# Kernel optimization log

Measured on AMD Instinct MI355X. Metric: run time of the kernel, lower is better.

Reference implementation:

```python
import jax, jax.numpy as jnp
import numpy as np

NB_STEPS = 50
ALPHA = 0.9
NUM_RNN_STEPS = 2
B = 4096
NUM_FEATURE = 100
IN_D = 5
HIDDEN = [64, 64, 64]
P1 = (1.1, 1.1, 1.5, 2.0, 2.5)   # IntegrandNN_outer_level powers
P2 = (1.5, 2.0, 2.5, 3.0, 3.5)   # IntegrandNN powers


def _cc(nb_steps):
    # Clenshaw-Curtis weights/steps, identical to UMNN's compute_cc_weights
    n = nb_steps
    i = np.arange(n + 1, dtype=np.float64).reshape(-1, 1)
    lam = np.cos(i @ i.T * np.pi / n)
    lam[:, 0] = 0.5
    lam[:, -1] *= 0.5
    lam = lam * 2.0 / n
    W = np.zeros(n + 1)
    even = np.arange(0, n + 1, 2)
    W[even] = 2.0 / (1.0 - even.astype(np.float64) ** 2)
    W[0] = 1.0
    ccw = (lam.T @ W).astype(np.float32)                         # [n+1]
    steps = np.cos(np.arange(n + 1) * np.pi / n).astype(np.float32)  # [n+1]
    return jnp.asarray(ccw), jnp.asarray(steps)

CC_W, CC_S = _cc(NB_STEPS)


def _mlp(xh, Ws, bs):
    # Linear+ReLU stack with ELU on the last layer (ReLU popped, ELU appended)
    h = xh
    for W, b in zip(Ws[:-1], bs[:-1]):
        h = jax.nn.relu(h @ W.T + b)
    return jax.nn.elu(h @ Ws[-1].T + bs[-1])


def _integrand(x, h, Ws, bs, Wf, powers):
    z = _mlp(jnp.concatenate([x, h], axis=1), Ws, bs) + 1.0      # [N,1], z >= 0
    feats = jnp.concatenate([z ** p for p in powers], axis=1)    # [N,5]
    return jax.nn.relu((1.0 / (feats + 1.0)) @ Wf.T)             # [N,1]


def _integrate(x0, xT, h, f):
    # ParallelNeuralIntegral forward: CC quadrature of f from x0 to xT
    Bn, S = x0.shape[0], NB_STEPS + 1
    X = x0[:, None, :] + (xT - x0)[:, None, :] * (CC_S[None, :, None] + 1.0) / 2.0  # [B,S,1]
    hs = jnp.broadcast_to(h[:, None, :], (Bn, S, h.shape[1])).reshape(-1, h.shape[1])
    dz = f(X.reshape(-1, 1), hs).reshape(Bn, S, 1)
    return (dz * CC_W[None, :, None]).sum(1) * (xT - x0) / 2.0   # [B,1]


def setup_inputs() -> dict:
    key = jax.random.key(0)
    ks = jax.random.split(key, 24)
    def lin(k, o, i):
        return jax.random.normal(k, (o, i), jnp.float32) / np.sqrt(i)
    d = {}
    d["x_"] = jax.random.normal(ks[0], (B, NUM_FEATURE), jnp.float32)
    d["h_"] = jax.random.normal(ks[1], (B, IN_D - 1), jnp.float32)
    d["log_weight"] = jnp.ones((1, NUM_FEATURE), jnp.float32)     # reset_parameters -> 1
    d["sigmoid_param"] = jnp.zeros((1,), jnp.float32)
    sizes = [IN_D] + HIDDEN + [1]
    for tag, base in (("f1", 2), ("f2", 12)):
        for li, (i, o) in enumerate(zip(sizes[:-1], sizes[1:])):
            d[f"{tag}_W{li}"] = lin(ks[base + 2 * li], o, i)
            d[f"{tag}_b{li}"] = jnp.zeros((o,), jnp.float32)
        d[f"{tag}_Wf"] = jnp.abs(lin(ks[base + 9], 1, 5))         # reset_params -> abs
    return d


def reference(x_, h_, log_weight, sigmoid_param,
              f1_W0, f1_b0, f1_W1, f1_b1, f1_W2, f1_b2, f1_W3, f1_b3, f1_Wf,
              f2_W0, f2_b0, f2_W1, f2_b1, f2_W2, f2_b2, f2_W3, f2_b3, f2_Wf):
    f1Ws = [f1_W0, f1_W1, f1_W2, f1_W3]; f1bs = [f1_b0, f1_b1, f1_b2, f1_b3]
    f2Ws = [f2_W0, f2_W1, f2_W2, f2_W3]; f2bs = [f2_b0, f2_b1, f2_b2, f2_b3]
    f1 = lambda x, h: _integrand(x, h, f1Ws, f1bs, f1_Wf, P1)
    f2 = lambda x, h: _integrand(x, h, f2Ws, f2bs, f2_Wf, P2)

    # modular function: linear to [B,1] then sum over dim 1 -> [B,1]
    xm = jnp.sum(x_ * log_weight[0], axis=1, keepdims=True)
    lam = jax.nn.sigmoid(sigmoid_param[0])

    I1 = jnp.zeros_like(xm)
    I2 = jnp.zeros_like(xm)
    out_first = None
    for _ in range(NUM_RNN_STEPS):
        x = (1.0 - lam) * xm + lam * I1
        x2 = (1.0 - lam) * xm + lam * I2
        out_first = f1(x2, h_)
        I1 = _integrate(jnp.zeros_like(x), x, h_, f1)
        xmax = jnp.max(x2) + 10.0
        xfinal = jnp.zeros_like(x) + xmax
        I2 = (1.0 / ALPHA) * _integrate(x2, xfinal, h_, f2)
    return I1, out_first, I2
```

## Files before the change

### kernel.cpp

```cpp
#include <hip/hip_runtime.h>
#include <math.h>

typedef _Float16 half8v __attribute__((ext_vector_type(8)));
typedef _Float16 half4v __attribute__((ext_vector_type(4)));
typedef _Float16 half2v __attribute__((ext_vector_type(2)));
typedef float float4v __attribute__((ext_vector_type(4)));

#define BB    4096
#define INV_ALPHA (1.0f/0.9f)

#define WS_CCW  0
#define WS_CCS  64
#define WS_LAM  128
#define WS_PM16 160
#define WS_PM   256
#define WS_XM   512
#define WS_X    (WS_XM + BB)
#define WS_X2   (WS_X + BB)
#define WS_H    16384
#define H_NET   8192
#define H_W2    4096
#define H_W0    16384
#define H_W3    20480

#if defined(__has_builtin)
#if __has_builtin(__builtin_amdgcn_rcpf)
#define FRCP(x) __builtin_amdgcn_rcpf(x)
#endif
#if __has_builtin(__builtin_amdgcn_exp2f)
#define FEXP2(x) __builtin_amdgcn_exp2f(x)
#endif
#if __has_builtin(__builtin_amdgcn_logf)
#define FLOG2(x) __builtin_amdgcn_logf(x)
#endif
#endif
#ifndef FRCP
#define FRCP(x) (1.0f / (x))
#endif
#ifndef FEXP2
#define FEXP2(x) exp2f(x)
#endif
#ifndef FLOG2
#define FLOG2(x) log2f(x)
#endif

__device__ __forceinline__ int swz(int row, int cb) {
    return (row << 6) + (((cb ^ (row & 7)) & 7) << 3);
}

__device__ __forceinline__ half4v pk_relu4(float4v c) {
#if defined(__has_builtin) && __has_builtin(__builtin_amdgcn_cvt_pkrtz)
    half2v a = __builtin_bit_cast(half2v,
        __builtin_amdgcn_cvt_pkrtz(fmaxf(c[0], 0.0f), fmaxf(c[1], 0.0f)));
    half2v b = __builtin_bit_cast(half2v,
        __builtin_amdgcn_cvt_pkrtz(fmaxf(c[2], 0.0f), fmaxf(c[3], 0.0f)));
    half4v o; o[0] = a[0]; o[1] = a[1]; o[2] = b[0]; o[3] = b[1];
    return o;
#else
    half4v o;
    o[0] = (_Float16)fmaxf(c[0], 0.0f); o[1] = (_Float16)fmaxf(c[1], 0.0f);
    o[2] = (_Float16)fmaxf(c[2], 0.0f); o[3] = (_Float16)fmaxf(c[3], 0.0f);
    return o;
#endif
}

__global__ void k_setup(const float* __restrict__ x_, const float* __restrict__ lw,
                        const float* __restrict__ sp,
                        const float* __restrict__ f1W0, const float* __restrict__ f1W1,
                        const float* __restrict__ f1W2, const float* __restrict__ f1W3,
                        const float* __restrict__ f2W0, const float* __restrict__ f2W1,
                        const float* __restrict__ f2W2, const float* __restrict__ f2W3,
                        float* __restrict__ ws, float* __restrict__ out) {
    _Float16* wh = (_Float16*)(ws + WS_H);
    const int blk = blockIdx.x, tid = threadIdx.x;
    if (blk < 256) {
        int wave = tid >> 6, lane = tid & 63;
        float vmax = -1e30f;
        for (int r = 0; r < 4; ++r) {
            int row = blk * 16 + wave * 4 + r;
            float v = 0.0f;
            for (int i = lane; i < 100; i += 64) v = fmaf(x_[row * 100 + i], lw[i], v);
            #pragma unroll
            for (int off = 32; off > 0; off >>= 1) v += __shfl_xor(v, off, 64);
            if (lane == 0) ws[WS_XM + row] = v;
            vmax = fmaxf(vmax, v);
        }
        __shared__ float sm[4];
        if (lane == 0) sm[wave] = vmax;
        __syncthreads();
        if (tid == 0)
            ws[WS_PM + blk] = fmaxf(fmaxf(sm[0], sm[1]), fmaxf(sm[2], sm[3]));
    } else if (blk < 272) {
        int t = (blk - 256) * 256 + tid;
        wh[t]                = (_Float16)f1W1[t];
        wh[H_W2 + t]         = (_Float16)f1W2[t];
        wh[H_NET + t]        = (_Float16)f2W1[t];
        wh[H_NET + H_W2 + t] = (_Float16)f2W2[t];
        if (t < 2048) {
            int j = t >> 5, k = t & 31;
            wh[H_W0 + t]        = (k < 5) ? (_Float16)f1W0[j * 5 + k] : (_Float16)0.0f;
            wh[H_W0 + 2048 + t] = (k < 5) ? (_Float16)f2W0[j * 5 + k] : (_Float16)0.0f;
        }
        if (t < 64) {
            wh[H_W3 + t]      = (_Float16)f1W3[t];
            wh[H_W3 + 64 + t] = (_Float16)f2W3[t];
        }
    } else if (blk == 272) {
        if (tid == 64) ws[WS_LAM] = 1.0f / (1.0f + expf(-sp[0]));
        if (tid <= 50) {
            int s = tid;
            ws[WS_CCS + s] = cospif((float)s / 50.0f);
            float acc = 0.0f;
            for (int a = 0; a <= 50; ++a) {
                float w;
                if (a == 0) w = 1.0f;
                else if ((a & 1) == 0) w = 2.0f / (1.0f - (float)(a * a));
                else continue;
                float l;
                if (s == 0) l = 0.5f;
                else {
                    int m = (a * s) % 100;
                    l = cospif((float)m / 50.0f);
                    if (s == 50) l *= 0.5f;
                }
                acc += l * 0.04f * w;
            }
            ws[WS_CCW + s] = acc;
        }
    } else {
        int t = (blk - 273) * 256 + tid;
        out[t < BB ? t : BB + t] = 0.0f;
    }
}

__global__ void k_pre(float* __restrict__ ws, float* __restrict__ out) {
    int b = blockIdx.x * 256 + threadIdx.x;
    float lam = ws[WS_LAM];
    float m = ws[WS_XM + b];
    float xv  = (1.0f - lam) * m + lam * out[b];
    float x2v = (1.0f - lam) * m + lam * out[2 * BB + b];
    ws[WS_X + b] = xv;
    ws[WS_X2 + b] = x2v;
    out[b] = 0.0f;
    out[2 * BB + b] = 0.0f;
    __shared__ float red[256];
    red[threadIdx.x] = x2v;
    __syncthreads();
    #pragma unroll
    for (int off = 128; off > 0; off >>= 1) {
        if (threadIdx.x < off)
            red[threadIdx.x] = fmaxf(red[threadIdx.x], red[threadIdx.x + off]);
        __syncthreads();
    }
    if (threadIdx.x == 0) ws[WS_PM16 + blockIdx.x] = red[0];
}

__global__ __launch_bounds__(64, 2) void k_int(
    int mode, float* __restrict__ ws, const float* __restrict__ h_,
    const float* __restrict__ f1b0, const float* __restrict__ f1b1,
    const float* __restrict__ f1b2, const float* __restrict__ f1b3,
    const float* __restrict__ f1Wf,
    const float* __restrict__ f2b0, const float* __restrict__ f2b1,
    const float* __restrict__ f2b2, const float* __restrict__ f2b3,
    const float* __restrict__ f2Wf,
    float* __restrict__ out)
{
    __shared__ _Float16 act[64 * 64];

    const int blk = blockIdx.x;
    const int lane = threadIdx.x;
    const int lo = lane & 15, q = lane >> 4;

    const float* xm = ws + WS_XM;
    const float* xarr = ws + WS_X;
    const float* x2arr = ws + WS_X2;
    const _Float16* wh = (const _Float16*)(ws + WS_H);
    const float lam = ws[WS_LAM];
    const float oml = 1.0f - lam;

    const bool is_of = (blk >= 2048);
    int base, w = 0, np;
    bool u2;
    if (is_of) {
        base = (blk - 2048) << 6; u2 = false; np = 1;
    } else {
        int g = blk >> 4;
        w = blk & 15;
        u2 = (g >= 64);
        base = (g & 63) << 6;
        np = (w < 3) ? 4 : 3;
    }

    const _Float16* W0h = wh + H_W0 + (u2 ? 2048 : 0);
    const _Float16* W1h = wh + (u2 ? H_NET : 0);
    const _Float16* W2h = W1h + H_W2;
    const _Float16* W3h = wh + H_W3 + (u2 ? 64 : 0);
    const float* B0 = u2 ? f2b0 : f1b0;
    const float* B1 = u2 ? f2b1 : f1b1;
    const float* B2 = u2 ? f2b2 : f1b2;
    const float* B3 = u2 ? f2b3 : f1b3;
    const float* WF = u2 ? f2Wf : f1Wf;
    const float p0 = u2 ? 1.5f : 1.1f;
    const float p1 = u2 ? 2.0f : 1.1f;
    const float p2 = u2 ? 2.5f : 1.5f;
    const float p3 = u2 ? 3.0f : 2.0f;
    const float p4 = u2 ? 3.5f : 2.5f;

    half8v A0w[4], A1w[4][2], A2w[4][2];
    float4v b0r[4], b1r[4], b2r[4];
    half4v w3r[4];
    #pragma unroll
    for (int m = 0; m < 4; ++m) {
        A0w[m]    = *(const half8v*)(W0h + (16 * m + lo) * 32 + q * 8);
        A1w[m][0] = *(const half8v*)(W1h + (16 * m + lo) * 64 + q * 8);
        A1w[m][1] = *(const half8v*)(W1h + (16 * m + lo) * 64 + 32 + q * 8);
        A2w[m][0] = *(const half8v*)(W2h + (16 * m + lo) * 64 + q * 8);
        A2w[m][1] = *(const half8v*)(W2h + (16 * m + lo) * 64 + 32 + q * 8);
        b0r[m] = *(const float4v*)(B0 + 16 * m + q * 4);
        b1r[m] = *(const float4v*)(B1 + 16 * m + q * 4);
        b2r[m] = *(const float4v*)(B2 + 16 * m + q * 4);
        w3r[m] = *(const half4v*)(W3h + 16 * m + 4 * q);
    }
    const float B3s = B3[0];
    const float wf0 = WF[0], wf1 = WF[1], wf2 = WF[2], wf3 = WF[3], wf4 = WF[4];

    float xr_r[4];
    float4 h4r[4];
    #pragma unroll
    for (int n = 0; n < 4; ++n) {
        int idx = base + 16 * n + lo;
        float v;
        if (is_of)      v = x2arr[idx];
        else if (mode)  v = u2 ? x2arr[idx] : xarr[idx];
        else            v = oml * xm[idx];
        xr_r[n] = v;
        h4r[n] = ((const float4*)h_)[idx];
    }

    float xmax = 0.0f;
    if (u2) {
        if (mode) {
            float v = (lane < 16) ? ws[WS_PM16 + lane] : -1e30f;
            #pragma unroll
            for (int off = 32; off > 0; off >>= 1) v = fmaxf(v, __shfl_xor(v, off, 64));
            xmax = v + 10.0f;
        } else {
            const float* pm = ws + WS_PM;
            float v = fmaxf(fmaxf(pm[lane], pm[lane + 64]),
                            fmaxf(pm[lane + 128], pm[lane + 192]));
            #pragma unroll
            for (int off = 32; off > 0; off >>= 1) v = fmaxf(v, __shfl_xor(v, off, 64));
            xmax = oml * v + 10.0f;
        }
    }

    float acc = 0.0f;

    #pragma clang loop unroll(disable)
    for (int p = 0; p < np; ++p) {
        const int s = w + 16 * p;
        float t = 0.0f, ccw_s = 0.0f;
        if (!is_of) {
            t = (ws[WS_CCS + s] + 1.0f) * 0.5f;
            ccw_s = ws[WS_CCW + s];
        }

        half8v Bf0[4];
        #pragma unroll
        for (int n = 0; n < 4; ++n) {
            float xin;
            if (is_of)   xin = xr_r[n];
            else if (u2) xin = fmaf(t, xmax - xr_r[n], xr_r[n]);
            else         xin = xr_r[n] * t;
            half8v e;
            e[0] = (_Float16)xin; e[1] = (_Float16)h4r[n].x; e[2] = (_Float16)h4r[n].y;
            e[3] = (_Float16)h4r[n].z; e[4] = (_Float16)h4r[n].w;
            e[5] = (_Float16)0.0f; e[6] = (_Float16)0.0f; e[7] = (_Float16)0.0f;
            half8v z;
            #pragma unroll
            for (int t2 = 0; t2 < 8; ++t2) z[t2] = (_Float16)0.0f;
            Bf0[n] = (q == 0) ? e : z;
        }

        #pragma unroll
        for (int m = 0; m < 4; ++m)
            #pragma unroll
            for (int n = 0; n < 4; ++n) {
                float4v c = __builtin_amdgcn_mfma_f32_16x16x32_f16(A0w[m], Bf0[n], b0r[m], 0, 0, 0);
                *(half4v*)(act + swz(16 * n + lo, 2 * m + (q >> 1)) + 4 * (q & 1)) = pk_relu4(c);
            }

        {
            half8v Bf[2][4];
            #pragma unroll
            for (int kb = 0; kb < 2; ++kb)
                #pragma unroll
                for (int n = 0; n < 4; ++n)
                    Bf[kb][n] = *(const half8v*)(act + swz(16 * n + lo, 4 * kb + q));
            #pragma unroll
            for (int m = 0; m < 4; ++m)
                #pragma unroll
                for (int n = 0; n < 4; ++n) {
                    float4v c = __builtin_amdgcn_mfma_f32_16x16x32_f16(A1w[m][0], Bf[0][n], b1r[m], 0, 0, 0);
                    c = __builtin_amdgcn_mfma_f32_16x16x32_f16(A1w[m][1], Bf[1][n], c, 0, 0, 0);
                    *(half4v*)(act + swz(16 * n + lo, 2 * m + (q >> 1)) + 4 * (q & 1)) = pk_relu4(c);
                }
        }

        float part[4] = {0.0f, 0.0f, 0.0f, 0.0f};
        {
            half8v Bf[2][4];
            #pragma unroll
            for (int kb = 0; kb < 2; ++kb)
                #pragma unroll
                for (int n = 0; n < 4; ++n)
                    Bf[kb][n] = *(const half8v*)(act + swz(16 * n + lo, 4 * kb + q));
            #pragma unroll
            for (int m = 0; m < 4; ++m)
                #pragma unroll
                for (int n = 0; n < 4; ++n) {
                    float4v c = __builtin_amdgcn_mfma_f32_16x16x32_f16(A2w[m][0], Bf[0][n], b2r[m], 0, 0, 0);
                    c = __builtin_amdgcn_mfma_f32_16x16x32_f16(A2w[m][1], Bf[1][n], c, 0, 0, 0);
                    #pragma unroll
                    for (int e = 0; e < 4; ++e)
                        part[n] = fmaf((float)w3r[m][e], fmaxf(c[e], 0.0f), part[n]);
                }
        }

        #pragma unroll
        for (int n = 0; n < 4; ++n) {
            part[n] += __shfl_xor(part[n], 16, 64);
            part[n] += __shfl_xor(part[n], 32, 64);
        }
        float y = B3s + (q == 0 ? part[0] : q == 1 ? part[1] : q == 2 ? part[2] : part[3]);

        if (y <= 0.0f) y = FEXP2(y * 1.44269504f) - 1.0f;
        float z = y + 1.0f;
        float lg = FLOG2(z);
        float g = wf0 * FRCP(FEXP2(p0 * lg) + 1.0f)
                + wf1 * FRCP(FEXP2(p1 * lg) + 1.0f)
                + wf2 * FRCP(FEXP2(p2 * lg) + 1.0f)
                + wf3 * FRCP(FEXP2(p3 * lg) + 1.0f)
                + wf4 * FRCP(FEXP2(p4 * lg) + 1.0f);
        float val = fmaxf(g, 0.0f);

        if (is_of) { out[BB + base + lane] = val; return; }
        acc += ccw_s * val;
    }

    const float x_l = (q == 0 ? xr_r[0] : q == 1 ? xr_r[1] : q == 2 ? xr_r[2] : xr_r[3]);
    if (!u2) {
        atomicAdd(out + base + lane, acc * x_l * 0.5f);
    } else {
        atomicAdd(out + 2 * BB + base + lane, acc * (xmax - x_l) * 0.5f * INV_ALPHA);
    }
}

extern "C" void kernel_launch(void* const* d_in, const int* in_sizes, int n_in,
                              void* d_out, int out_size, void* d_ws, size_t ws_size,
                              hipStream_t stream) {
    const float* x_  = (const float*)d_in[0];
    const float* h_  = (const float*)d_in[1];
    const float* lw  = (const float*)d_in[2];
    const float* sp  = (const float*)d_in[3];
    const float* f1W0 = (const float*)d_in[4];   const float* f1b0 = (const float*)d_in[5];
    const float* f1W1 = (const float*)d_in[6];   const float* f1b1 = (const float*)d_in[7];
    const float* f1W2 = (const float*)d_in[8];   const float* f1b2 = (const float*)d_in[9];
    const float* f1W3 = (const float*)d_in[10];  const float* f1b3 = (const float*)d_in[11];
    const float* f1Wf = (const float*)d_in[12];
    const float* f2W0 = (const float*)d_in[13];  const float* f2b0 = (const float*)d_in[14];
    const float* f2W1 = (const float*)d_in[15];  const float* f2b1 = (const float*)d_in[16];
    const float* f2W2 = (const float*)d_in[17];  const float* f2b2 = (const float*)d_in[18];
    const float* f2W3 = (const float*)d_in[19];  const float* f2b3 = (const float*)d_in[20];
    const float* f2Wf = (const float*)d_in[21];
    float* out = (float*)d_out;
    float* ws  = (float*)d_ws;

    k_setup<<<305, 256, 0, stream>>>(x_, lw, sp,
                                     f1W0, f1W1, f1W2, f1W3,
                                     f2W0, f2W1, f2W2, f2W3, ws, out);
    k_int<<<2048, 64, 0, stream>>>(0, ws, h_,
        f1b0, f1b1, f1b2, f1b3, f1Wf, f2b0, f2b1, f2b2, f2b3, f2Wf, out);
    k_pre<<<16, 256, 0, stream>>>(ws, out);
    k_int<<<2112, 64, 0, stream>>>(1, ws, h_,
        f1b0, f1b1, f1b2, f1b3, f1Wf, f2b0, f2b1, f2b2, f2b3, f2Wf, out);
}
```

Before: 144.0 us.

## Stream weights per pass instead of register-caching, flatten work to per-step tiles

The kernel stops holding every MLP weight fragment in registers for the block's lifetime. It now loads A fragments and biases from global/L2 just before each layer's MFMAs, and raises the launch bound to 4 waves per SIMD so occupancy can rise. Work is redistributed so each 64-thread block processes two flat (tile, quadrature step) units, 3264 per integrand, instead of 3-4 strided steps. Each unit atomically adds its weighted contribution using unsafeAtomicAdd. The trade-off is many more weight reloads and far more atomics in exchange for lower register pressure and better latency hiding.

```diff
diff --git a/kernel.cpp b/kernel.cpp
--- a/kernel.cpp
+++ b/kernel.cpp
@@ -8,6 +8,9 @@
 
 #define BB    4096
 #define INV_ALPHA (1.0f/0.9f)
+#define NPASS1 3264
+#define NPASS2 6528
+#define OFBASE 6528
 
 #define WS_CCW  0
 #define WS_CCS  64
@@ -42,6 +45,12 @@
 #endif
 #ifndef FLOG2
 #define FLOG2(x) log2f(x)
+#endif
+
+#if defined(__HIP_PLATFORM_AMD__)
+#define ATOMIC_ADD_F32(p, v) unsafeAtomicAdd((p), (v))
+#else
+#define ATOMIC_ADD_F32(p, v) atomicAdd((p), (v))
 #endif
 
 __device__ __forceinline__ int swz(int row, int cb) {
@@ -155,7 +164,7 @@
     if (threadIdx.x == 0) ws[WS_PM16 + blockIdx.x] = red[0];
 }
 
-__global__ __launch_bounds__(64, 2) void k_int(
+__global__ __launch_bounds__(64, 4) void k_int(
     int mode, float* __restrict__ ws, const float* __restrict__ h_,
     const float* __restrict__ f1b0, const float* __restrict__ f1b1,
     const float* __restrict__ f1b2, const float* __restrict__ f1b3,
@@ -167,7 +176,6 @@
 {
     __shared__ _Float16 act[64 * 64];
 
-    const int blk = blockIdx.x;
     const int lane = threadIdx.x;
     const int lo = lane & 15, q = lane >> 4;
 
@@ -178,103 +186,70 @@
     const float lam = ws[WS_LAM];
     const float oml = 1.0f - lam;
 
-    const bool is_of = (blk >= 2048);
-    int base, w = 0, np;
-    bool u2;
-    if (is_of) {
-        base = (blk - 2048) << 6; u2 = false; np = 1;
+    float xmax;
+    if (mode) {
+        float v = (lane < 16) ? ws[WS_PM16 + lane] : -1e30f;
+        #pragma unroll
+        for (int off = 32; off > 0; off >>= 1) v = fmaxf(v, __shfl_xor(v, off, 64));
+        xmax = v + 10.0f;
     } else {
-        int g = blk >> 4;
-        w = blk & 15;
-        u2 = (g >= 64);
-        base = (g & 63) << 6;
-        np = (w < 3) ? 4 : 3;
+        const float* pm = ws + WS_PM;
+        float v = fmaxf(fmaxf(pm[lane], pm[lane + 64]),
+                        fmaxf(pm[lane + 128], pm[lane + 192]));
+        #pragma unroll
+        for (int off = 32; off > 0; off >>= 1) v = fmaxf(v, __shfl_xor(v, off, 64));
+        xmax = oml * v + 10.0f;
     }
 
-    const _Float16* W0h = wh + H_W0 + (u2 ? 2048 : 0);
-    const _Float16* W1h = wh + (u2 ? H_NET : 0);
-    const _Float16* W2h = W1h + H_W2;
-    const _Float16* W3h = wh + H_W3 + (u2 ? 64 : 0);
-    const float* B0 = u2 ? f2b0 : f1b0;
-    const float* B1 = u2 ? f2b1 : f1b1;
-    const float* B2 = u2 ? f2b2 : f1b2;
-    const float* B3 = u2 ? f2b3 : f1b3;
-    const float* WF = u2 ? f2Wf : f1Wf;
-    const float p0 = u2 ? 1.5f : 1.1f;
-    const float p1 = u2 ? 2.0f : 1.1f;
-    const float p2 = u2 ? 2.5f : 1.5f;
-    const float p3 = u2 ? 3.0f : 2.0f;
-    const float p4 = u2 ? 3.5f : 2.5f;
-
-    half8v A0w[4], A1w[4][2], A2w[4][2];
-    float4v b0r[4], b1r[4], b2r[4];
-    half4v w3r[4];
-    #pragma unroll
-    for (int m = 0; m < 4; ++m) {
-        A0w[m]    = *(const half8v*)(W0h + (16 * m + lo) * 32 + q * 8);
-        A1w[m][0] = *(const half8v*)(W1h + (16 * m + lo) * 64 + q * 8);
-        A1w[m][1] = *(const half8v*)(W1h + (16 * m + lo) * 64 + 32 + q * 8);
-        A2w[m][0] = *(const half8v*)(W2h + (16 * m + lo) * 64 + q * 8);
-        A2w[m][1] = *(const half8v*)(W2h + (16 * m + lo) * 64 + 32 + q * 8);
-        b0r[m] = *(const float4v*)(B0 + 16 * m + q * 4);
-        b1r[m] = *(const float4v*)(B1 + 16 * m + q * 4);
-        b2r[m] = *(const float4v*)(B2 + 16 * m + q * 4);
-        w3r[m] = *(const half4v*)(W3h + 16 * m + 4 * q);
-    }
-    const float B3s = B3[0];
-    const float wf0 = WF[0], wf1 = WF[1], wf2 = WF[2], wf3 = WF[3], wf4 = WF[4];
-
-    float xr_r[4];
-    float4 h4r[4];
-    #pragma unroll
-    for (int n = 0; n < 4; ++n) {
-        int idx = base + 16 * n + lo;
-        float v;
-        if (is_of)      v = x2arr[idx];
-        else if (mode)  v = u2 ? x2arr[idx] : xarr[idx];
-        else            v = oml * xm[idx];
-        xr_r[n] = v;
-        h4r[n] = ((const float4*)h_)[idx];
-    }
-
-    float xmax = 0.0f;
-    if (u2) {
-        if (mode) {
-            float v = (lane < 16) ? ws[WS_PM16 + lane] : -1e30f;
-            #pragma unroll
-            for (int off = 32; off > 0; off >>= 1) v = fmaxf(v, __shfl_xor(v, off, 64));
-            xmax = v + 10.0f;
-        } else {
-            const float* pm = ws + WS_PM;
-            float v = fmaxf(fmaxf(pm[lane], pm[lane + 64]),
-                            fmaxf(pm[lane + 128], pm[lane + 192]));
-            #pragma unroll
-            for (int off = 32; off > 0; off >>= 1) v = fmaxf(v, __shfl_xor(v, off, 64));
-            xmax = oml * v + 10.0f;
-        }
-    }
-
-    float acc = 0.0f;
-
     #pragma clang loop unroll(disable)
-    for (int p = 0; p < np; ++p) {
-        const int s = w + 16 * p;
+    for (int pp = 0; pp < 2; ++pp) {
+        const int P = blockIdx.x + pp * (int)gridDim.x;
+        const bool is_of = (P >= OFBASE);
+        const bool u2 = (!is_of) && (P >= NPASS1);
+        const int Pn = is_of ? 0 : (u2 ? P - NPASS1 : P);
+        const int g = is_of ? (P - OFBASE) : (Pn / 51);
+        const int s = Pn - g * 51;
+        const int base = g << 6;
+
+        const _Float16* W0h = wh + H_W0 + (u2 ? 2048 : 0);
+        const _Float16* W1h = wh + (u2 ? H_NET : 0);
+        const _Float16* W2h = W1h + H_W2;
+        const _Float16* W3h = wh + H_W3 + (u2 ? 64 : 0);
+        const float* B0 = u2 ? f2b0 : f1b0;
+        const float* B1 = u2 ? f2b1 : f1b1;
+        const float* B2 = u2 ? f2b2 : f1b2;
+        const float* B3 = u2 ? f2b3 : f1b3;
+        const float* WF = u2 ? f2Wf : f1Wf;
+        const float p0 = u2 ? 1.5f : 1.1f;
+        const float p1 = u2 ? 2.0f : 1.1f;
+        const float p2 = u2 ? 2.5f : 1.5f;
+        const float p3 = u2 ? 3.0f : 2.0f;
+        const float p4 = u2 ? 3.5f : 2.5f;
+
         float t = 0.0f, ccw_s = 0.0f;
         if (!is_of) {
             t = (ws[WS_CCS + s] + 1.0f) * 0.5f;
             ccw_s = ws[WS_CCW + s];
         }
 
+        float xr_r[4];
         half8v Bf0[4];
         #pragma unroll
         for (int n = 0; n < 4; ++n) {
+            int idx = base + 16 * n + lo;
+            float v;
+            if (is_of)      v = x2arr[idx];
+            else if (mode)  v = u2 ? x2arr[idx] : xarr[idx];
+            else            v = oml * xm[idx];
+            xr_r[n] = v;
+            float4 hr = ((const float4*)h_)[idx];
             float xin;
-            if (is_of)   xin = xr_r[n];
-            else if (u2) xin = fmaf(t, xmax - xr_r[n], xr_r[n]);
-            else         xin = xr_r[n] * t;
+            if (is_of)   xin = v;
+            else if (u2) xin = fmaf(t, xmax - v, v);
+            else         xin = v * t;
             half8v e;
-            e[0] = (_Float16)xin; e[1] = (_Float16)h4r[n].x; e[2] = (_Float16)h4r[n].y;
-            e[3] = (_Float16)h4r[n].z; e[4] = (_Float16)h4r[n].w;
+            e[0] = (_Float16)xin; e[1] = (_Float16)hr.x; e[2] = (_Float16)hr.y;
+            e[3] = (_Float16)hr.z; e[4] = (_Float16)hr.w;
             e[5] = (_Float16)0.0f; e[6] = (_Float16)0.0f; e[7] = (_Float16)0.0f;
             half8v z;
             #pragma unroll
@@ -283,12 +258,15 @@
         }
 
         #pragma unroll
-        for (int m = 0; m < 4; ++m)
+        for (int m = 0; m < 4; ++m) {
+            half8v Af = *(const half8v*)(W0h + (16 * m + lo) * 32 + q * 8);
+            float4v bb = *(const float4v*)(B0 + 16 * m + q * 4);
             #pragma unroll
             for (int n = 0; n < 4; ++n) {
-                float4v c = __builtin_amdgcn_mfma_f32_16x16x32_f16(A0w[m], Bf0[n], b0r[m], 0, 0, 0);
+                float4v c = __builtin_amdgcn_mfma_f32_16x16x32_f16(Af, Bf0[n], bb, 0, 0, 0);
                 *(half4v*)(act + swz(16 * n + lo, 2 * m + (q >> 1)) + 4 * (q & 1)) = pk_relu4(c);
             }
+        }
 
         {
             half8v Bf[2][4];
@@ -298,13 +276,17 @@
                 for (int n = 0; n < 4; ++n)
                     Bf[kb][n] = *(const half8v*)(act + swz(16 * n + lo, 4 * kb + q));
             #pragma unroll
-            for (int m = 0; m < 4; ++m)
+            for (int m = 0; m < 4; ++m) {
+                half8v A0 = *(const half8v*)(W1h + (16 * m + lo) * 64 + q * 8);
+                half8v A1 = *(const half8v*)(W1h + (16 * m + lo) * 64 + 32 + q * 8);
+                float4v bb = *(const float4v*)(B1 + 16 * m + q * 4);
                 #pragma unroll
                 for (int n = 0; n < 4; ++n) {
-                    float4v c = __builtin_amdgcn_mfma_f32_16x16x32_f16(A1w[m][0], Bf[0][n], b1r[m], 0, 0, 0);
-                    c = __builtin_amdgcn_mfma_f32_16x16x32_f16(A1w[m][1], Bf[1][n], c, 0, 0, 0);
+                    float4v c = __builtin_amdgcn_mfma_f32_16x16x32_f16(A0, Bf[0][n], bb, 0, 0, 0);
+                    c = __builtin_amdgcn_mfma_f32_16x16x32_f16(A1, Bf[1][n], c, 0, 0, 0);
                     *(half4v*)(act + swz(16 * n + lo, 2 * m + (q >> 1)) + 4 * (q & 1)) = pk_relu4(c);
                 }
+            }
         }
 
         float part[4] = {0.0f, 0.0f, 0.0f, 0.0f};
@@ -316,15 +298,20 @@
                 for (int n = 0; n < 4; ++n)
                     Bf[kb][n] = *(const half8v*)(act + swz(16 * n + lo, 4 * kb + q));
             #pragma unroll
-            for (int m = 0; m < 4; ++m)
+            for (int m = 0; m < 4; ++m) {
+                half8v A0 = *(const half8v*)(W2h + (16 * m + lo) * 64 + q * 8);
+                half8v A1 = *(const half8v*)(W2h + (16 * m + lo) * 64 + 32 + q * 8);
+                float4v bb = *(const float4v*)(B2 + 16 * m + q * 4);
+                half4v w3 = *(const half4v*)(W3h + 16 * m + 4 * q);
                 #pragma unroll
                 for (int n = 0; n < 4; ++n) {
-                    float4v c = __builtin_amdgcn_mfma_f32_16x16x32_f16(A2w[m][0], Bf[0][n], b2r[m], 0, 0, 0);
-                    c = __builtin_amdgcn_mfma_f32_16x16x32_f16(A2w[m][1], Bf[1][n], c, 0, 0, 0);
+                    float4v c = __builtin_amdgcn_mfma_f32_16x16x32_f16(A0, Bf[0][n], bb, 0, 0, 0);
+                    c = __builtin_amdgcn_mfma_f32_16x16x32_f16(A1, Bf[1][n], c, 0, 0, 0);
                     #pragma unroll
                     for (int e = 0; e < 4; ++e)
-                        part[n] = fmaf((float)w3r[m][e], fmaxf(c[e], 0.0f), part[n]);
+                        part[n] = fmaf((float)w3[e], fmaxf(c[e], 0.0f), part[n]);
                 }
+            }
         }
 
         #pragma unroll
@@ -332,27 +319,27 @@
             part[n] += __shfl_xor(part[n], 16, 64);
             part[n] += __shfl_xor(part[n], 32, 64);
         }
-        float y = B3s + (q == 0 ? part[0] : q == 1 ? part[1] : q == 2 ? part[2] : part[3]);
+        float y = (q == 0 ? part[0] : q == 1 ? part[1] : q == 2 ? part[2] : part[3]);
+        y += B3[0];
 
         if (y <= 0.0f) y = FEXP2(y * 1.44269504f) - 1.0f;
         float z = y + 1.0f;
         float lg = FLOG2(z);
-        float g = wf0 * FRCP(FEXP2(p0 * lg) + 1.0f)
-                + wf1 * FRCP(FEXP2(p1 * lg) + 1.0f)
-                + wf2 * FRCP(FEXP2(p2 * lg) + 1.0f)
-                + wf3 * FRCP(FEXP2(p3 * lg) + 1.0f)
-                + wf4 * FRCP(FEXP2(p4 * lg) + 1.0f);
-        float val = fmaxf(g, 0.0f);
-
-        if (is_of) { out[BB + base + lane] = val; return; }
-        acc += ccw_s * val;
-    }
-
-    const float x_l = (q == 0 ? xr_r[0] : q == 1 ? xr_r[1] : q == 2 ? xr_r[2] : xr_r[3]);
-    if (!u2) {
-        atomicAdd(out + base + lane, acc * x_l * 0.5f);
-    } else {
-        atomicAdd(out + 2 * BB + base + lane, acc * (xmax - x_l) * 0.5f * INV_ALPHA);
+        float gg = WF[0] * FRCP(FEXP2(p0 * lg) + 1.0f)
+                 + WF[1] * FRCP(FEXP2(p1 * lg) + 1.0f)
+                 + WF[2] * FRCP(FEXP2(p2 * lg) + 1.0f)
+                 + WF[3] * FRCP(FEXP2(p3 * lg) + 1.0f)
+                 + WF[4] * FRCP(FEXP2(p4 * lg) + 1.0f);
+        float val = fmaxf(gg, 0.0f);
+
+        if (is_of) { out[BB + base + lane] = val; continue; }
+
+        const float x_l = (q == 0 ? xr_r[0] : q == 1 ? xr_r[1] : q == 2 ? xr_r[2] : xr_r[3]);
+        if (!u2)
+            ATOMIC_ADD_F32(out + base + lane, ccw_s * val * x_l * 0.5f);
+        else
+            ATOMIC_ADD_F32(out + 2 * BB + base + lane,
+                           ccw_s * val * (xmax - x_l) * 0.5f * INV_ALPHA);
     }
 }
 
@@ -379,9 +366,9 @@
     k_setup<<<305, 256, 0, stream>>>(x_, lw, sp,
                                      f1W0, f1W1, f1W2, f1W3,
                                      f2W0, f2W1, f2W2, f2W3, ws, out);
-    k_int<<<2048, 64, 0, stream>>>(0, ws, h_,
+    k_int<<<NPASS2 / 2, 64, 0, stream>>>(0, ws, h_,
         f1b0, f1b1, f1b2, f1b3, f1Wf, f2b0, f2b1, f2b2, f2b3, f2Wf, out);
     k_pre<<<16, 256, 0, stream>>>(ws, out);
-    k_int<<<2112, 64, 0, stream>>>(1, ws, h_,
+    k_int<<<(NPASS2 + 64) / 2, 64, 0, stream>>>(1, ws, h_,
         f1b0, f1b1, f1b2, f1b3, f1Wf, f2b0, f2b1, f2b2, f2b3, f2Wf, out);
 }
```

New measurement: 148.2 us. 2.9% more time.

## Drop k_pre launch by recomputing RNN inputs and max inside k_int

Applied to the files above, without the earlier changes.

Removes the intermediate k_pre kernel. The first k_int pass now accumulates its integrals into zeroed workspace buffers, which k_setup clears with extra blocks. The second pass recomputes x and x2 from xm and those buffers, and each u2 block redundantly scans all 4096 elements to find the max. Atomics are now issued once per quadrature point using unsafeAtomicAdd, instead of once per block after the loop. This trades a kernel launch and its sync for redundant per-block max scans and three to four times as many atomics.

```diff
diff --git a/kernel.cpp b/kernel.cpp
--- a/kernel.cpp
+++ b/kernel.cpp
@@ -12,11 +12,10 @@
 #define WS_CCW  0
 #define WS_CCS  64
 #define WS_LAM  128
-#define WS_PM16 160
 #define WS_PM   256
 #define WS_XM   512
-#define WS_X    (WS_XM + BB)
-#define WS_X2   (WS_X + BB)
+#define WS_A01  (WS_XM + BB)
+#define WS_A02  (WS_XM + 2*BB)
 #define WS_H    16384
 #define H_NET   8192
 #define H_W2    4096
@@ -42,6 +41,12 @@
 #endif
 #ifndef FLOG2
 #define FLOG2(x) log2f(x)
+#endif
+
+#if defined(__HIP_PLATFORM_AMD__)
+#define ATOMIC_ADD_F32(p, v) unsafeAtomicAdd((p), (v))
+#else
+#define ATOMIC_ADD_F32(p, v) atomicAdd((p), (v))
 #endif
 
 __device__ __forceinline__ int swz(int row, int cb) {
@@ -129,30 +134,9 @@
         }
     } else {
         int t = (blk - 273) * 256 + tid;
-        out[t < BB ? t : BB + t] = 0.0f;
-    }
-}
-
-__global__ void k_pre(float* __restrict__ ws, float* __restrict__ out) {
-    int b = blockIdx.x * 256 + threadIdx.x;
-    float lam = ws[WS_LAM];
-    float m = ws[WS_XM + b];
-    float xv  = (1.0f - lam) * m + lam * out[b];
-    float x2v = (1.0f - lam) * m + lam * out[2 * BB + b];
-    ws[WS_X + b] = xv;
-    ws[WS_X2 + b] = x2v;
-    out[b] = 0.0f;
-    out[2 * BB + b] = 0.0f;
-    __shared__ float red[256];
-    red[threadIdx.x] = x2v;
-    __syncthreads();
-    #pragma unroll
-    for (int off = 128; off > 0; off >>= 1) {
-        if (threadIdx.x < off)
-            red[threadIdx.x] = fmaxf(red[threadIdx.x], red[threadIdx.x + off]);
-        __syncthreads();
-    }
-    if (threadIdx.x == 0) ws[WS_PM16 + blockIdx.x] = red[0];
+        if (t < 8192) out[t < BB ? t : BB + t] = 0.0f;
+        else          ws[WS_A01 + (t - 8192)] = 0.0f;
+    }
 }
 
 __global__ __launch_bounds__(64, 2) void k_int(
@@ -172,8 +156,8 @@
     const int lo = lane & 15, q = lane >> 4;
 
     const float* xm = ws + WS_XM;
-    const float* xarr = ws + WS_X;
-    const float* x2arr = ws + WS_X2;
+    const float* a01 = ws + WS_A01;
+    const float* a02 = ws + WS_A02;
     const _Float16* wh = (const _Float16*)(ws + WS_H);
     const float lam = ws[WS_LAM];
     const float oml = 1.0f - lam;
@@ -230,9 +214,10 @@
     for (int n = 0; n < 4; ++n) {
         int idx = base + 16 * n + lo;
         float v;
-        if (is_of)      v = x2arr[idx];
-        else if (mode)  v = u2 ? x2arr[idx] : xarr[idx];
-        else            v = oml * xm[idx];
+        if (mode == 0)   v = oml * xm[idx];
+        else if (is_of)  v = fmaf(lam, a02[idx], oml * xm[idx]);
+        else if (u2)     v = fmaf(lam, a02[idx], oml * xm[idx]);
+        else             v = fmaf(lam, a01[idx], oml * xm[idx]);
         xr_r[n] = v;
         h4r[n] = ((const float4*)h_)[idx];
     }
@@ -240,10 +225,12 @@
     float xmax = 0.0f;
     if (u2) {
         if (mode) {
-            float v = (lane < 16) ? ws[WS_PM16 + lane] : -1e30f;
-            #pragma unroll
-            for (int off = 32; off > 0; off >>= 1) v = fmaxf(v, __shfl_xor(v, off, 64));
-            xmax = v + 10.0f;
+            float vm = -1e30f;
+            for (int i = lane; i < BB; i += 64)
+                vm = fmaxf(vm, fmaf(lam, a02[i], oml * xm[i]));
+            #pragma unroll
+            for (int off = 32; off > 0; off >>= 1) vm = fmaxf(vm, __shfl_xor(vm, off, 64));
+            xmax = vm + 10.0f;
         } else {
             const float* pm = ws + WS_PM;
             float v = fmaxf(fmaxf(pm[lane], pm[lane + 64]),
@@ -253,8 +240,6 @@
             xmax = oml * v + 10.0f;
         }
     }
-
-    float acc = 0.0f;
 
     #pragma clang loop unroll(disable)
     for (int p = 0; p < np; ++p) {
@@ -337,22 +322,23 @@
         if (y <= 0.0f) y = FEXP2(y * 1.44269504f) - 1.0f;
         float z = y + 1.0f;
         float lg = FLOG2(z);
-        float g = wf0 * FRCP(FEXP2(p0 * lg) + 1.0f)
-                + wf1 * FRCP(FEXP2(p1 * lg) + 1.0f)
-                + wf2 * FRCP(FEXP2(p2 * lg) + 1.0f)
-                + wf3 * FRCP(FEXP2(p3 * lg) + 1.0f)
-                + wf4 * FRCP(FEXP2(p4 * lg) + 1.0f);
-        float val = fmaxf(g, 0.0f);
-
-        if (is_of) { out[BB + base + lane] = val; return; }
-        acc += ccw_s * val;
-    }
-
-    const float x_l = (q == 0 ? xr_r[0] : q == 1 ? xr_r[1] : q == 2 ? xr_r[2] : xr_r[3]);
-    if (!u2) {
-        atomicAdd(out + base + lane, acc * x_l * 0.5f);
-    } else {
-        atomicAdd(out + 2 * BB + base + lane, acc * (xmax - x_l) * 0.5f * INV_ALPHA);
+        float gg = wf0 * FRCP(FEXP2(p0 * lg) + 1.0f)
+                 + wf1 * FRCP(FEXP2(p1 * lg) + 1.0f)
+                 + wf2 * FRCP(FEXP2(p2 * lg) + 1.0f)
+                 + wf3 * FRCP(FEXP2(p3 * lg) + 1.0f)
+                 + wf4 * FRCP(FEXP2(p4 * lg) + 1.0f);
+        float val = fmaxf(gg, 0.0f);
+
+        if (is_of) { out[BB + base + lane] = val; continue; }
+
+        const float x_l = (q == 0 ? xr_r[0] : q == 1 ? xr_r[1] : q == 2 ? xr_r[2] : xr_r[3]);
+        if (!u2) {
+            float* dst = mode ? (out + base + lane) : (float*)(a01 + base + lane);
+            ATOMIC_ADD_F32(dst, ccw_s * val * x_l * 0.5f);
+        } else {
+            float* dst = mode ? (out + 2 * BB + base + lane) : (float*)(a02 + base + lane);
+            ATOMIC_ADD_F32(dst, ccw_s * val * (xmax - x_l) * 0.5f * INV_ALPHA);
+        }
     }
 }
 
@@ -376,12 +362,11 @@
     float* out = (float*)d_out;
     float* ws  = (float*)d_ws;
 
-    k_setup<<<305, 256, 0, stream>>>(x_, lw, sp,
+    k_setup<<<337, 256, 0, stream>>>(x_, lw, sp,
                                      f1W0, f1W1, f1W2, f1W3,
                                      f2W0, f2W1, f2W2, f2W3, ws, out);
     k_int<<<2048, 64, 0, stream>>>(0, ws, h_,
         f1b0, f1b1, f1b2, f1b3, f1Wf, f2b0, f2b1, f2b2, f2b3, f2Wf, out);
-    k_pre<<<16, 256, 0, stream>>>(ws, out);
     k_int<<<2112, 64, 0, stream>>>(1, ws, h_,
         f1b0, f1b1, f1b2, f1b3, f1Wf, f2b0, f2b1, f2b2, f2b3, f2Wf, out);
 }
```

Result: slower. 148.1 us (+2.8%).
